# Kernel optimization log

Hardware: AMD Instinct MI355X
Metric: run time of the kernel (lower is better)

The kernel has to match this reference:

```python
import jax, jax.numpy as jnp
import numpy as np

B, C, H, W = 2, 192, 64, 64
NHEADS = 8


def setup_inputs() -> dict:
    key = jax.random.key(0)
    ks = jax.random.split(key, 6)
    L = H * W
    return {
        "x": jax.random.normal(ks[0], (B, C, H, W), dtype=jnp.float32),
        "mask": jax.random.normal(ks[1], (B, L, L), dtype=jnp.float32),
        "w_qkv": jax.random.normal(ks[2], (3 * C, C), dtype=jnp.float32) * (1.0 / np.sqrt(C)),
        "b_qkv": jax.random.normal(ks[3], (3 * C,), dtype=jnp.float32) * 0.02,
        "w_proj": jax.random.normal(ks[4], (C, C), dtype=jnp.float32) * (1.0 / np.sqrt(C)),
        "b_proj": jax.random.normal(ks[5], (C,), dtype=jnp.float32) * 0.02,
        "num_heads": NHEADS,
    }


def reference(x, mask, w_qkv, b_qkv, w_proj, b_proj, num_heads):
    b, c, h, w = x.shape
    L = h * w
    hd = c // num_heads  # head dim
    # 1x1 conv == per-pixel linear over channels
    qkv = jnp.einsum('bchw,oc->bohw', x, w_qkv) + b_qkv[None, :, None, None]
    q, k, v = jnp.split(qkv, 3, axis=1)  # each [b, c, h, w]

    def to_heads(t):
        # b (head hd) h w -> b head (h w) hd
        return t.reshape(b, num_heads, hd, L).transpose(0, 1, 3, 2)

    q, k, v = to_heads(q), to_heads(k), to_heads(v)
    scale = num_heads ** (-0.5)  # NOTE: original scales by num_heads, not head_dim
    attn = jnp.einsum('bnld,bnmd->bnlm', q, k) * scale + mask[:, None, :, :]
    attn = jax.nn.softmax(attn, axis=-1)
    out = jnp.einsum('bnlm,bnmd->bnld', attn, v)  # [b, head, L, hd]
    # b head L hd -> b (head hd) h w
    out = out.transpose(0, 1, 3, 2).reshape(b, c, h, w)
    out = jnp.einsum('bchw,oc->bohw', out, w_proj) + b_proj[None, :, None, None]
    return out
```

## Files before the change

### kernel.cpp

```cpp
#include <hip/hip_runtime.h>

#define B_  2
#define C_  192
#define L_  4096
#define NH_ 8
#define HD_ 24
#define C3_ 576
#define KV_ 64
#define NT_ (L_ / KV_)

typedef _Float16 f16;
typedef __attribute__((ext_vector_type(8))) f16 f16x8;
typedef __attribute__((ext_vector_type(16))) float f32x16;

#define L2E_ 1.4426950408889634f

__device__ __forceinline__ int pk2(float a, float b) {
    union { __fp16 h __attribute__((ext_vector_type(2))); int i; } u;
    u.h = __builtin_amdgcn_cvt_pkrtz(a, b);
    return u.i;
}
__device__ __forceinline__ int pk2_rte(float a, float b) {
    union { f16 h[2]; int i; } u;
    u.h[0] = (f16)a; u.h[1] = (f16)b;
    return u.i;
}
__device__ __forceinline__ float ex2(float x) {
    float r;
    asm("v_exp_f32 %0, %1" : "=v"(r) : "v"(x));
    return r;
}

union Frag { f16x8 v; int i[4]; };

#define MFMA32(A, Bx, Cc) __builtin_amdgcn_mfma_f32_32x32x16_f16((A), (Bx), (Cc), 0, 0, 0)

__device__ __forceinline__ void gload4(const void* g, void* lds) {
    typedef const unsigned int __attribute__((address_space(1))) as1u;
    typedef unsigned int __attribute__((address_space(3))) as3u;
    __builtin_amdgcn_global_load_lds((as1u*)g,
                                     (as3u*)(unsigned int)(unsigned long long)lds,
                                     4, 0, 0);
}

#define WAITV(N) asm volatile("s_waitcnt vmcnt(" #N ")" ::: "memory")
#define BAR()    __builtin_amdgcn_s_barrier()

__global__ __launch_bounds__(256) void lin_qkv(const float* __restrict__ a,
                                               const float* __restrict__ w,
                                               const float* __restrict__ bias,
                                               unsigned int* __restrict__ q2,
                                               unsigned int* __restrict__ k2,
                                               unsigned short* __restrict__ v16) {
    __shared__ float wl[8][C_];
    const int og  = blockIdx.x;
    const int b   = blockIdx.y >> 4;
    const int lt  = blockIdx.y & 15;
    const int tid = threadIdx.x;

    for (int e = tid; e < 8 * C_; e += 256) wl[e / C_][e % C_] = w[og * 8 * C_ + e];
    __syncthreads();

    const int l = lt * 256 + tid;
    float acc[8];
#pragma unroll
    for (int j = 0; j < 8; ++j) acc[j] = bias[og * 8 + j];

    const float* ap = a + (size_t)b * C_ * L_ + l;
#pragma unroll 2
    for (int c = 0; c < C_; ++c) {
        const float xv = ap[(size_t)c * L_];
#pragma unroll
        for (int j = 0; j < 8; ++j) acc[j] = fmaf(wl[j][c], xv, acc[j]);
    }

    const float qscale = 0.35355339059327373f * L2E_;
    if (og < 48) {
        unsigned int* dst = (og < 24) ? q2 : k2;
        const int og_ = (og < 24) ? og : og - 24;
        const float sc = (og < 24) ? qscale : 1.f;
        const int h = og_ / 3, j0 = (og_ % 3) * 4;
        unsigned int* p = dst + ((size_t)(b * NH_ + h) * 12 + j0) * L_ + l;
#pragma unroll
        for (int j = 0; j < 4; ++j)
            p[(size_t)j * L_] = pk2_rte(acc[2 * j] * sc, acc[2 * j + 1] * sc);
    } else {
        const int og_ = og - 48;
        const int h = og_ / 3, d0 = (og_ % 3) * 8;
        unsigned short* p = v16 + ((size_t)(b * NH_ + h) * 24 + d0) * L_ + l;
#pragma unroll
        for (int j = 0; j < 8; ++j) {
            union { f16 hf; unsigned short us; } cv;
            cv.hf = (f16)acc[j];
            p[(size_t)j * L_] = cv.us;
        }
    }
}

__global__ __launch_bounds__(256) void lin_kernel(const float* __restrict__ a,
                                                  const float* __restrict__ w,
                                                  const float* __restrict__ bias,
                                                  float* __restrict__ out, int OC) {
    __shared__ float wl[8][C_];
    const int og  = blockIdx.x;
    const int b   = blockIdx.y >> 4;
    const int lt  = blockIdx.y & 15;
    const int tid = threadIdx.x;

    for (int e = tid; e < 8 * C_; e += 256) wl[e / C_][e % C_] = w[og * 8 * C_ + e];
    __syncthreads();

    const int l = lt * 256 + tid;
    float acc[8];
#pragma unroll
    for (int j = 0; j < 8; ++j) acc[j] = bias[og * 8 + j];

    const float* ap = a + (size_t)b * C_ * L_ + l;
#pragma unroll 2
    for (int c = 0; c < C_; ++c) {
        const float xv = ap[(size_t)c * L_];
#pragma unroll
        for (int j = 0; j < 8; ++j) acc[j] = fmaf(wl[j][c], xv, acc[j]);
    }

    float* op = out + ((size_t)b * OC + og * 8) * L_ + l;
#pragma unroll
    for (int j = 0; j < 8; ++j) op[(size_t)j * L_] = acc[j];
}

__global__ __launch_bounds__(256) void attn_mfma(const unsigned int* __restrict__ q2,
                                                 const unsigned int* __restrict__ k2,
                                                 const unsigned short* __restrict__ v16,
                                                 const float* __restrict__ mask,
                                                 float* __restrict__ out) {
    const int tid  = threadIdx.x;
    const int lane = tid & 63;
    const int wid  = tid >> 6;
    const int hi   = lane >> 5;
    const int lq   = lane & 31;
    const int bid  = blockIdx.x;
    const int h    = bid >> 6;
    const int b    = (bid >> 5) & 1;
    const int qt   = bid & 31;
    const int qrow = qt * 128 + wid * 32 + lq;

    __shared__ int k_lds[4][16][64];
    __shared__ int v_lds[4][32][32];

#pragma unroll
    for (int bf = 0; bf < 4; ++bf)
#pragma unroll
        for (int i = 0; i < 4; ++i) k_lds[bf][12 + i][lane] = 0;

    const unsigned int*   qb = q2  + (size_t)(b * NH_ + h) * 12 * L_;
    const unsigned int*   kb = k2  + (size_t)(b * NH_ + h) * 12 * L_;
    const unsigned short* vb = v16 + (size_t)(b * NH_ + h) * 24 * L_;
    const float* mrow = mask + ((size_t)b * L_ + qrow) * L_;

    int bq[8];
#pragma unroll
    for (int s = 0; s < 2; ++s)
#pragma unroll
        for (int t = 0; t < 4; ++t) {
            const int dpq = 8 * s + 4 * hi + t;
            bq[s * 4 + t] = (dpq < 12) ? qb[(size_t)dpq * L_ + qrow] : 0;
        }

    const unsigned int*   kg[3];
    const unsigned short* vg[3];
    int ls_off[3];
#pragma unroll
    for (int i = 0; i < 3; ++i) {
        const int e = i * 256 + tid;
        kg[i]     = kb + (size_t)(e >> 6) * L_ + (e & 63);
        const int d = e >> 5, slot = e & 31;
        vg[i]     = vb + (size_t)d * L_ + 2 * (slot ^ d);
        ls_off[i] = i * 256 + 64 * wid;
    }

#define STAGE(BF, KK) do {                                                    \
    _Pragma("unroll")                                                         \
    for (int i_ = 0; i_ < 3; ++i_) {                                          \
        gload4(kg[i_] + (KK), &k_lds[BF][0][0] + ls_off[i_]);                 \
        gload4(vg[i_] + (KK), &v_lds[BF][0][0] + ls_off[i_]);                 \
    } } while (0)

#define MLOAD(MD, KK) do {                                                    \
    const float4* mb_ = (const float4*)(mrow + (KK));                         \
    _Pragma("unroll")                                                         \
    for (int u_ = 0; u_ < 2; ++u_)                                            \
        _Pragma("unroll")                                                     \
        for (int q_ = 0; q_ < 4; ++q_)                                        \
            MD[u_ * 4 + q_] = mb_[8 * u_ + 2 * q_ + hi];                      \
    } while (0)

#define PVSTEP(BF, CU, U) do {                                                \
    int w1[4], w2[4], s1[4], s2[4];                                           \
    _Pragma("unroll")                                                         \
    for (int q_ = 0; q_ < 4; ++q_) {                                          \
        w1[q_] = pk2(CU[4 * q_], CU[4 * q_ + 1]);                             \
        w2[q_] = pk2(CU[4 * q_ + 2], CU[4 * q_ + 3]);                         \
    }                                                                         \
    _Pragma("unroll")                                                         \
    for (int q_ = 0; q_ < 4; ++q_) {                                          \
        s1[q_] = __shfl_xor(w1[q_], 32);                                      \
        s2[q_] = __shfl_xor(w2[q_], 32);                                      \
    }                                                                         \
    _Pragma("unroll")                                                         \
    for (int s_ = 0; s_ < 2; ++s_) {                                          \
        const int qq_ = 2 * s_ + hi;                                          \
        Frag pb, va;                                                          \
        pb.i[0] = hi ? s1[qq_] : w1[qq_];                                     \
        pb.i[1] = hi ? s2[qq_] : w2[qq_];                                     \
        pb.i[2] = hi ? w1[qq_] : s1[qq_];                                     \
        pb.i[3] = hi ? w2[qq_] : s2[qq_];                                     \
        _Pragma("unroll")                                                     \
        for (int t_ = 0; t_ < 4; ++t_)                                        \
            va.i[t_] = v_lds[BF][lq][(16 * U + 8 * s_ + 4 * hi + t_) ^ lq];   \
        __builtin_amdgcn_s_setprio(1);                                        \
        o = MFMA32(va.v, pb.v, o);                                            \
        __builtin_amdgcn_s_setprio(0);                                        \
    } } while (0)

#define COMPUTE(BF, MC) do {                                                  \
    f32x16 c0, c1;                                                            \
    c0[0]  = MC[0].x * L2E_; c0[1]  = MC[0].y * L2E_;                         \
    c0[2]  = MC[0].z * L2E_; c0[3]  = MC[0].w * L2E_;                         \
    c0[4]  = MC[1].x * L2E_; c0[5]  = MC[1].y * L2E_;                         \
    c0[6]  = MC[1].z * L2E_; c0[7]  = MC[1].w * L2E_;                         \
    c0[8]  = MC[2].x * L2E_; c0[9]  = MC[2].y * L2E_;                         \
    c0[10] = MC[2].z * L2E_; c0[11] = MC[2].w * L2E_;                         \
    c0[12] = MC[3].x * L2E_; c0[13] = MC[3].y * L2E_;                         \
    c0[14] = MC[3].z * L2E_; c0[15] = MC[3].w * L2E_;                         \
    c1[0]  = MC[4].x * L2E_; c1[1]  = MC[4].y * L2E_;                         \
    c1[2]  = MC[4].z * L2E_; c1[3]  = MC[4].w * L2E_;                         \
    c1[4]  = MC[5].x * L2E_; c1[5]  = MC[5].y * L2E_;                         \
    c1[6]  = MC[5].z * L2E_; c1[7]  = MC[5].w * L2E_;                         \
    c1[8]  = MC[6].x * L2E_; c1[9]  = MC[6].y * L2E_;                         \
    c1[10] = MC[6].z * L2E_; c1[11] = MC[6].w * L2E_;                         \
    c1[12] = MC[7].x * L2E_; c1[13] = MC[7].y * L2E_;                         \
    c1[14] = MC[7].z * L2E_; c1[15] = MC[7].w * L2E_;                         \
    Frag qf0, qf1, ka0, ka1;                                                  \
    _Pragma("unroll")                                                         \
    for (int t_ = 0; t_ < 4; ++t_) { qf0.i[t_] = bq[t_]; qf1.i[t_] = bq[4 + t_]; } \
    _Pragma("unroll")                                                         \
    for (int t_ = 0; t_ < 4; ++t_) {                                          \
        ka0.i[t_] = k_lds[BF][4 * hi + t_][lq];                               \
        ka1.i[t_] = k_lds[BF][8 + 4 * hi + t_][lq];                           \
    }                                                                         \
    __builtin_amdgcn_s_setprio(1);                                            \
    c0 = MFMA32(ka0.v, qf0.v, c0);                                            \
    c0 = MFMA32(ka1.v, qf1.v, c0);                                            \
    __builtin_amdgcn_s_setprio(0);                                            \
    _Pragma("unroll")                                                         \
    for (int t_ = 0; t_ < 4; ++t_) {                                          \
        ka0.i[t_] = k_lds[BF][4 * hi + t_][32 + lq];                          \
        ka1.i[t_] = k_lds[BF][8 + 4 * hi + t_][32 + lq];                      \
    }                                                                         \
    __builtin_amdgcn_s_setprio(1);                                            \
    c1 = MFMA32(ka0.v, qf0.v, c1);                                            \
    c1 = MFMA32(ka1.v, qf1.v, c1);                                            \
    __builtin_amdgcn_s_setprio(0);                                            \
    float pmax = c0[0];                                                       \
    _Pragma("unroll")                                                         \
    for (int i_ = 1; i_ < 16; ++i_) pmax = fmaxf(pmax, c0[i_]);               \
    _Pragma("unroll")                                                         \
    for (int i_ = 0; i_ < 16; ++i_) pmax = fmaxf(pmax, c1[i_]);               \
    pmax = fmaxf(pmax, __shfl_xor(pmax, 32));                                 \
    if (!__all((int)(pmax <= mrun + 11.5415603f))) {                          \
        const float newm_ = fmaxf(mrun, pmax);                                \
        const float r_ = ex2(mrun - newm_);                                   \
        srun *= r_;                                                           \
        _Pragma("unroll")                                                     \
        for (int i_ = 0; i_ < 16; ++i_) o[i_] *= r_;                          \
        mrun = newm_;                                                         \
    }                                                                         \
    float ls = 0.f;                                                           \
    _Pragma("unroll")                                                         \
    for (int i_ = 0; i_ < 16; ++i_) { c0[i_] = ex2(c0[i_] - mrun); ls += c0[i_]; } \
    _Pragma("unroll")                                                         \
    for (int i_ = 0; i_ < 16; ++i_) { c1[i_] = ex2(c1[i_] - mrun); ls += c1[i_]; } \
    ls += __shfl_xor(ls, 32);                                                 \
    srun += ls;                                                               \
    PVSTEP(BF, c0, 0);                                                        \
    PVSTEP(BF, c1, 1);                                                        \
    } while (0)

    f32x16 o;
#pragma unroll
    for (int i = 0; i < 16; ++i) o[i] = 0.f;
    float mrun = -1e30f, srun = 0.f;
    float4 ma[8], mb[8];

    STAGE(0, 0);
    MLOAD(ma, 0);
    STAGE(1, KV_);

#pragma clang loop unroll(disable)
    for (int t = 0; t < NT_ - 4; t += 4) {
        const int kk = t * KV_;
        MLOAD(mb, kk + 1 * KV_); STAGE(2, kk + 2 * KV_); WAITV(20); BAR(); COMPUTE(0, ma);
        MLOAD(ma, kk + 2 * KV_); STAGE(3, kk + 3 * KV_); WAITV(20); BAR(); COMPUTE(1, mb);
        MLOAD(mb, kk + 3 * KV_); STAGE(0, kk + 4 * KV_); WAITV(20); BAR(); COMPUTE(2, ma);
        MLOAD(ma, kk + 4 * KV_); STAGE(1, kk + 5 * KV_); WAITV(20); BAR(); COMPUTE(3, mb);
    }
    {
        const int kk = (NT_ - 4) * KV_;
        MLOAD(mb, kk + 1 * KV_); STAGE(2, kk + 2 * KV_); WAITV(20); BAR(); COMPUTE(0, ma);
        MLOAD(ma, kk + 2 * KV_); STAGE(3, kk + 3 * KV_); WAITV(20); BAR(); COMPUTE(1, mb);
        MLOAD(mb, kk + 3 * KV_);                         WAITV(14); BAR(); COMPUTE(2, ma);
                                                         WAITV(0);  BAR(); COMPUTE(3, mb);
    }

    const float inv = 1.f / srun;
    float* op = out + ((size_t)b * C_ + h * HD_) * L_ + qrow;
#pragma unroll
    for (int i = 0; i < 16; ++i) {
        const int d = (i & 3) + 8 * (i >> 2) + 4 * hi;
        if (d < HD_) op[(size_t)d * L_] = o[i] * inv;
    }
#undef STAGE
#undef MLOAD
#undef PVSTEP
#undef COMPUTE
}

extern "C" void kernel_launch(void* const* d_in, const int* in_sizes, int n_in,
                              void* d_out, int out_size, void* d_ws, size_t ws_size,
                              hipStream_t stream) {
    const float* x      = (const float*)d_in[0];
    const float* mask   = (const float*)d_in[1];
    const float* w_qkv  = (const float*)d_in[2];
    const float* b_qkv  = (const float*)d_in[3];
    const float* w_proj = (const float*)d_in[4];
    const float* b_proj = (const float*)d_in[5];
    float* out = (float*)d_out;

    unsigned int*   q2  = (unsigned int*)d_ws;
    unsigned int*   k2  = q2 + (size_t)B_ * NH_ * 12 * L_;
    unsigned short* v16 = (unsigned short*)(k2 + (size_t)B_ * NH_ * 12 * L_);
    float* ws_att = (float*)(v16 + (size_t)B_ * NH_ * 24 * L_);

    lin_qkv<<<dim3(72, 32), 256, 0, stream>>>(x, w_qkv, b_qkv, q2, k2, v16);
    attn_mfma<<<dim3(512), 256, 0, stream>>>(q2, k2, v16, mask, ws_att);
    lin_kernel<<<dim3(24, 32), 256, 0, stream>>>(ws_att, w_proj, b_proj, out, C_);
}
```

Baseline: 371.6 us.

## Split attention KV range across two blocks and merge with log-sum-exp combine

Splits each query tile's key/value range into two halves handled by separate blocks, doubling the grid from 512 to 1024 blocks. Partial outputs are stored as fp16 along with a per-row log-sum-exp, and a new combine kernel merges them before the projection. The pipeline also changes from a 4-buffer vmcnt-based scheme to a simpler double buffer with __syncthreads. This targets under-occupancy of the GPU's CUs. In exchange it adds a kernel launch, extra partial-result traffic, fp16 rounding of the partials, and possibly weaker latency hiding in the simpler pipeline.

```diff
diff --git a/kernel.cpp b/kernel.cpp
--- a/kernel.cpp
+++ b/kernel.cpp
@@ -7,7 +7,9 @@
 #define HD_ 24
 #define C3_ 576
 #define KV_ 64
-#define NT_ (L_ / KV_)
+#define NSPL_ 2
+#define LSPL_ (L_ / NSPL_)
+#define NT2_ (LSPL_ / KV_)
 
 typedef _Float16 f16;
 typedef __attribute__((ext_vector_type(8))) f16 f16x8;
@@ -28,6 +30,11 @@
 __device__ __forceinline__ float ex2(float x) {
     float r;
     asm("v_exp_f32 %0, %1" : "=v"(r) : "v"(x));
+    return r;
+}
+__device__ __forceinline__ float lg2(float x) {
+    float r;
+    asm("v_log_f32 %0, %1" : "=v"(r) : "v"(x));
     return r;
 }
 
@@ -42,9 +49,6 @@
                                      (as3u*)(unsigned int)(unsigned long long)lds,
                                      4, 0, 0);
 }
-
-#define WAITV(N) asm volatile("s_waitcnt vmcnt(" #N ")" ::: "memory")
-#define BAR()    __builtin_amdgcn_s_barrier()
 
 __global__ __launch_bounds__(256) void lin_qkv(const float* __restrict__ a,
                                                const float* __restrict__ w,
@@ -132,25 +136,30 @@
                                                  const unsigned int* __restrict__ k2,
                                                  const unsigned short* __restrict__ v16,
                                                  const float* __restrict__ mask,
-                                                 float* __restrict__ out) {
+                                                 unsigned short* __restrict__ po,
+                                                 float* __restrict__ pms) {
     const int tid  = threadIdx.x;
     const int lane = tid & 63;
     const int wid  = tid >> 6;
     const int hi   = lane >> 5;
     const int lq   = lane & 31;
     const int bid  = blockIdx.x;
-    const int h    = bid >> 6;
-    const int b    = (bid >> 5) & 1;
-    const int qt   = bid & 31;
+    const int sp   = bid >> 9;
+    const int r    = bid & 511;
+    const int h    = r >> 6;
+    const int b    = (r >> 5) & 1;
+    const int qt   = r & 31;
     const int qrow = qt * 128 + wid * 32 + lq;
-
-    __shared__ int k_lds[4][16][64];
-    __shared__ int v_lds[4][32][32];
-
-#pragma unroll
-    for (int bf = 0; bf < 4; ++bf)
-#pragma unroll
-        for (int i = 0; i < 4; ++i) k_lds[bf][12 + i][lane] = 0;
+    const int kv0  = sp * LSPL_;
+
+    __shared__ int k_lds[2][16][64];
+    __shared__ int v_lds[2][32][32];
+
+    {
+        const int rr = 12 + (tid >> 6), cc = tid & 63;
+        k_lds[0][rr][cc] = 0;
+        k_lds[1][rr][cc] = 0;
+    }
 
     const unsigned int*   qb = q2  + (size_t)(b * NH_ + h) * 12 * L_;
     const unsigned int*   kb = k2  + (size_t)(b * NH_ + h) * 12 * L_;
@@ -290,39 +299,70 @@
 #pragma unroll
     for (int i = 0; i < 16; ++i) o[i] = 0.f;
     float mrun = -1e30f, srun = 0.f;
-    float4 ma[8], mb[8];
-
-    STAGE(0, 0);
-    MLOAD(ma, 0);
-    STAGE(1, KV_);
-
-#pragma clang loop unroll(disable)
-    for (int t = 0; t < NT_ - 4; t += 4) {
-        const int kk = t * KV_;
-        MLOAD(mb, kk + 1 * KV_); STAGE(2, kk + 2 * KV_); WAITV(20); BAR(); COMPUTE(0, ma);
-        MLOAD(ma, kk + 2 * KV_); STAGE(3, kk + 3 * KV_); WAITV(20); BAR(); COMPUTE(1, mb);
-        MLOAD(mb, kk + 3 * KV_); STAGE(0, kk + 4 * KV_); WAITV(20); BAR(); COMPUTE(2, ma);
-        MLOAD(ma, kk + 4 * KV_); STAGE(1, kk + 5 * KV_); WAITV(20); BAR(); COMPUTE(3, mb);
-    }
-    {
-        const int kk = (NT_ - 4) * KV_;
-        MLOAD(mb, kk + 1 * KV_); STAGE(2, kk + 2 * KV_); WAITV(20); BAR(); COMPUTE(0, ma);
-        MLOAD(ma, kk + 2 * KV_); STAGE(3, kk + 3 * KV_); WAITV(20); BAR(); COMPUTE(1, mb);
-        MLOAD(mb, kk + 3 * KV_);                         WAITV(14); BAR(); COMPUTE(2, ma);
-                                                         WAITV(0);  BAR(); COMPUTE(3, mb);
+    float4 mc[8], mn[8];
+
+    STAGE(0, kv0);
+    MLOAD(mc, kv0);
+    __syncthreads();
+
+    for (int t = 0; t < NT2_; t += 2) {
+        const int kk = kv0 + t * KV_;
+        STAGE(1, kk + KV_);
+        MLOAD(mn, kk + KV_);
+        COMPUTE(0, mc);
+        __syncthreads();
+        if (t + 2 < NT2_) {
+            STAGE(0, kk + 2 * KV_);
+            MLOAD(mc, kk + 2 * KV_);
+        }
+        COMPUTE(1, mn);
+        __syncthreads();
     }
 
     const float inv = 1.f / srun;
-    float* op = out + ((size_t)b * C_ + h * HD_) * L_ + qrow;
+    const float lse = mrun + lg2(srun);
+    unsigned short* pob = po + ((size_t)((sp * B_ + b) * NH_ + h) * HD_) * L_ + qrow;
 #pragma unroll
     for (int i = 0; i < 16; ++i) {
         const int d = (i & 3) + 8 * (i >> 2) + 4 * hi;
-        if (d < HD_) op[(size_t)d * L_] = o[i] * inv;
-    }
+        if (d < HD_) {
+            union { __fp16 hf; unsigned short us; } cv;
+            cv.hf = (__fp16)(o[i] * inv);
+            pob[(size_t)d * L_] = cv.us;
+        }
+    }
+    if (hi == 0)
+        pms[((size_t)(sp * B_ + b) * NH_ + h) * L_ + qrow] = lse;
 #undef STAGE
 #undef MLOAD
 #undef PVSTEP
 #undef COMPUTE
+}
+
+__global__ __launch_bounds__(256) void combine_kernel(const unsigned short* __restrict__ po,
+                                                      const float* __restrict__ pms,
+                                                      float* __restrict__ att) {
+    const int qrow = blockIdx.x * 256 + threadIdx.x;
+    const int h    = blockIdx.y;
+    const int b    = blockIdx.z;
+
+    const float l0 = pms[((size_t)(0 * B_ + b) * NH_ + h) * L_ + qrow];
+    const float l1 = pms[((size_t)(1 * B_ + b) * NH_ + h) * L_ + qrow];
+    const float lm = fmaxf(l0, l1);
+    const float w0 = ex2(l0 - lm);
+    const float w1 = ex2(l1 - lm);
+    const float inv = 1.f / (w0 + w1);
+
+    const unsigned short* p0 = po + ((size_t)((0 * B_ + b) * NH_ + h) * HD_) * L_ + qrow;
+    const unsigned short* p1 = po + ((size_t)((1 * B_ + b) * NH_ + h) * HD_) * L_ + qrow;
+    float* op = att + ((size_t)b * C_ + h * HD_) * L_ + qrow;
+#pragma unroll
+    for (int d = 0; d < HD_; ++d) {
+        union { unsigned short us; __fp16 hf; } a, c;
+        a.us = p0[(size_t)d * L_];
+        c.us = p1[(size_t)d * L_];
+        op[(size_t)d * L_] = ((float)a.hf * w0 + (float)c.hf * w1) * inv;
+    }
 }
 
 extern "C" void kernel_launch(void* const* d_in, const int* in_sizes, int n_in,
@@ -339,9 +379,12 @@
     unsigned int*   q2  = (unsigned int*)d_ws;
     unsigned int*   k2  = q2 + (size_t)B_ * NH_ * 12 * L_;
     unsigned short* v16 = (unsigned short*)(k2 + (size_t)B_ * NH_ * 12 * L_);
-    float* ws_att = (float*)(v16 + (size_t)B_ * NH_ * 24 * L_);
+    unsigned short* po  = v16 + (size_t)B_ * NH_ * HD_ * L_;
+    float* pms    = (float*)(po + (size_t)NSPL_ * B_ * NH_ * HD_ * L_);
+    float* ws_att = pms + (size_t)NSPL_ * B_ * NH_ * L_;
 
     lin_qkv<<<dim3(72, 32), 256, 0, stream>>>(x, w_qkv, b_qkv, q2, k2, v16);
-    attn_mfma<<<dim3(512), 256, 0, stream>>>(q2, k2, v16, mask, ws_att);
+    attn_mfma<<<dim3(512 * NSPL_), 256, 0, stream>>>(q2, k2, v16, mask, po, pms);
+    combine_kernel<<<dim3(16, NH_, B_), 256, 0, stream>>>(po, pms, ws_att);
     lin_kernel<<<dim3(24, 32), 256, 0, stream>>>(ws_att, w_proj, b_proj, out, C_);
 }
```

Result: faster. 345.0 us (-7.1%).
